# Kernel tuning notes

Hardware: AMD Instinct MI355X
Metric: run time of the kernel (lower is better)

The kernel has to match this reference:

```python
import jax, jax.numpy as jnp
import numpy as np
import math

D_MODEL = 768
N_HEAD = 12
SEQ_LEN = 2048
BATCH = 4


def setup_inputs() -> dict:
    key = jax.random.key(0)
    ks = jax.random.split(key, 5)
    x = jax.random.normal(ks[0], (BATCH, SEQ_LEN, D_MODEL), dtype=jnp.float32)
    s = 1.0 / math.sqrt(D_MODEL)
    W_attn = jax.random.uniform(ks[1], (D_MODEL, 3 * D_MODEL), minval=-s, maxval=s, dtype=jnp.float32)
    b_attn = jax.random.uniform(ks[2], (3 * D_MODEL,), minval=-s, maxval=s, dtype=jnp.float32)
    W_proj = jax.random.uniform(ks[3], (D_MODEL, D_MODEL), minval=-s, maxval=s, dtype=jnp.float32)
    b_proj = jax.random.uniform(ks[4], (D_MODEL,), minval=-s, maxval=s, dtype=jnp.float32)
    return {"x": x, "W_attn": W_attn, "b_attn": b_attn, "W_proj": W_proj, "b_proj": b_proj}


def reference(x, W_attn, b_attn, W_proj, b_proj):
    B, T, C = x.shape
    H = N_HEAD
    hd = C // H
    qkv = x @ W_attn + b_attn  # [B,T,3C]
    q, k, v = jnp.split(qkv, 3, axis=-1)
    # [B,H,T,hd]
    q = q.reshape(B, T, H, hd).transpose(0, 2, 1, 3)
    k = k.reshape(B, T, H, hd).transpose(0, 2, 1, 3)
    v = v.reshape(B, T, H, hd).transpose(0, 2, 1, 3)
    att = jnp.einsum('bhqd,bhkd->bhqk', q, k) * (1.0 / math.sqrt(hd))  # [B,H,T,T]
    causal = jnp.tril(jnp.ones((T, T), dtype=bool))
    att = jnp.where(causal[None, None, :, :], att, -jnp.inf)
    att = jax.nn.softmax(att, axis=-1)
    # attn_pdrop = resid_pdrop = 0.0 -> dropout is identity
    y = jnp.einsum('bhqk,bhkd->bhqd', att, v)  # [B,H,T,hd]
    y = y.transpose(0, 2, 1, 3).reshape(B, T, C)
    return y @ W_proj + b_proj
```

## Files before the change

kernel.cpp:

```cpp
#include <hip/hip_runtime.h>
#include <hip/hip_bf16.h>
#include <math.h>

#define D_MODEL 768
#define N_HEAD  12
#define SEQ     2048
#define BATCH   4
#define HD      64
#define BH      (BATCH*N_HEAD)

typedef __bf16 bf16;
typedef __bf16 bf16x4 __attribute__((ext_vector_type(4)));
typedef __bf16 bf16x8 __attribute__((ext_vector_type(8)));
typedef float  f32x4  __attribute__((ext_vector_type(4)));
typedef float  f32x16 __attribute__((ext_vector_type(16)));
typedef unsigned int u32;

__device__ __forceinline__ f32x4 mfma16(bf16x8 a, bf16x8 b, f32x4 c) {
    return __builtin_amdgcn_mfma_f32_16x16x32_bf16(a, b, c, 0, 0, 0);
}
__device__ __forceinline__ f32x16 mfma32(bf16x8 a, bf16x8 b, f32x16 c) {
    return __builtin_amdgcn_mfma_f32_32x32x16_bf16(a, b, c, 0, 0, 0);
}

__device__ __forceinline__ void gload16(const void* g, void* l) {
    __builtin_amdgcn_global_load_lds((const __attribute__((address_space(1))) u32*)g,
                                     (__attribute__((address_space(3))) u32*)l, 16, 0, 0);
}

__global__ void cvt_bf16(const float* __restrict__ in, bf16* __restrict__ out, int n) {
    int i = (blockIdx.x * blockDim.x + threadIdx.x) * 4;
    if (i < n) {
        float4 v = *(const float4*)(in + i);
        bf16x4 o;
        o[0] = (bf16)v.x; o[1] = (bf16)v.y; o[2] = (bf16)v.z; o[3] = (bf16)v.w;
        *(bf16x4*)(out + i) = o;
    }
}

__global__ __launch_bounds__(256)
void transpose_cvt(const float* __restrict__ in, bf16* __restrict__ out, int R, int C) {
    __shared__ float tile[64][65];
    int tid = threadIdx.x;
    int tr = blockIdx.y * 64, tc = blockIdx.x * 64;
    int r0 = tid >> 4, c0 = (tid & 15) * 4;
    #pragma unroll
    for (int i = 0; i < 4; ++i) {
        float4 v = *(const float4*)&in[(long)(tr + r0 + i * 16) * C + tc + c0];
        tile[r0 + i * 16][c0 + 0] = v.x;
        tile[r0 + i * 16][c0 + 1] = v.y;
        tile[r0 + i * 16][c0 + 2] = v.z;
        tile[r0 + i * 16][c0 + 3] = v.w;
    }
    __syncthreads();
    int orr = (tid & 15) * 4;
    #pragma unroll
    for (int i = 0; i < 4; ++i) {
        int oc = (tid >> 4) + i * 16;
        bf16x4 o;
        #pragma unroll
        for (int j = 0; j < 4; ++j) o[j] = (bf16)tile[orr + j][oc];
        *(bf16x4*)&out[(long)(tc + oc) * R + tr + orr] = o;
    }
}

template<int MODE>
__global__ __launch_bounds__(256)
void gemm_bt(const bf16* __restrict__ A, const bf16* __restrict__ Bt,
             const float* __restrict__ bias,
             bf16* __restrict__ qo, bf16* __restrict__ ko, bf16* __restrict__ vto,
             float* __restrict__ outf,
             int M, int N, int K) {
    __shared__ bf16 As[128 * 32];
    __shared__ bf16 Bs[128 * 32];
    int tid = threadIdx.x;
    int wave = tid >> 6, lane = tid & 63;
    int wr = wave >> 1, wc = wave & 1;
    int lq = lane >> 4, lc = lane & 15;
    int mbase = blockIdx.x * 128, nbase = blockIdx.y * 128;
    int srow = wave * 32 + (lane >> 2), scol = (lane & 3) * 8;
    const bf16* aS = A  + (long)(mbase + srow) * K + scol;
    const bf16* bS = Bt + (long)(nbase + srow) * K + scol;
    char* AsB = (char*)As + wave * 2048;
    char* BsB = (char*)Bs + wave * 2048;
    f32x4 acc[4][4] = {};
    for (int kt = 0; kt < K; kt += 32) {
        gload16(aS + kt,                AsB);
        gload16(aS + 16 * (long)K + kt, AsB + 1024);
        gload16(bS + kt,                BsB);
        gload16(bS + 16 * (long)K + kt, BsB + 1024);
        __syncthreads();
        bf16x8 af[4], bfr[4];
        #pragma unroll
        for (int mf = 0; mf < 4; ++mf)
            af[mf]  = *(const bf16x8*)((char*)As + (wr * 64 + mf * 16 + lc) * 64 + lq * 16);
        #pragma unroll
        for (int nf = 0; nf < 4; ++nf)
            bfr[nf] = *(const bf16x8*)((char*)Bs + (wc * 64 + nf * 16 + lc) * 64 + lq * 16);
        __builtin_amdgcn_s_setprio(1);
        #pragma unroll
        for (int mf = 0; mf < 4; ++mf)
            #pragma unroll
            for (int nf = 0; nf < 4; ++nf)
                acc[mf][nf] = mfma16(af[mf], bfr[nf], acc[mf][nf]);
        __builtin_amdgcn_s_setprio(0);
        __syncthreads();
    }
    #pragma unroll
    for (int mf = 0; mf < 4; ++mf) {
        #pragma unroll
        for (int nf = 0; nf < 4; ++nf) {
            int n = nbase + wc * 64 + nf * 16 + lc;
            float bv = bias[n];
            int m0 = mbase + wr * 64 + mf * 16 + lq * 4;
            if (MODE == 0) {
                int sect = n / 768, cc = n % 768;
                int h = cc >> 6, d = cc & 63;
                int b = m0 >> 11, t0 = m0 & 2047;
                long bh = (long)b * N_HEAD + h;
                if (sect == 0) {
                    #pragma unroll
                    for (int r = 0; r < 4; ++r)
                        qo[(bh * SEQ + t0 + r) * HD + d] = (bf16)((acc[mf][nf][r] + bv) * 0.18033688f);
                } else if (sect == 1) {
                    #pragma unroll
                    for (int r = 0; r < 4; ++r)
                        ko[(bh * SEQ + t0 + r) * HD + d] = (bf16)(acc[mf][nf][r] + bv);
                } else {
                    bf16x4 o;
                    #pragma unroll
                    for (int r = 0; r < 4; ++r) o[r] = (bf16)(acc[mf][nf][r] + bv);
                    *(bf16x4*)&vto[(bh * HD + d) * SEQ + t0] = o;
                }
            } else {
                #pragma unroll
                for (int r = 0; r < 4; ++r)
                    outf[(long)(m0 + r) * N + n] = acc[mf][nf][r] + bv;
            }
        }
    }
}

__global__ __launch_bounds__(256, 4)
void attn_kernel(const bf16* __restrict__ qg, const bf16* __restrict__ kg,
                 const bf16* __restrict__ vtg, bf16* __restrict__ yg) {
    __shared__ __align__(16) bf16 KV[4][64 * 64];
    int tid = threadIdx.x;
    int wave = tid >> 6, lane = tid & 63;
    int q5 = lane & 31, h = lane >> 5;
    int bh = blockIdx.x;
    int tau = gridDim.y - 1 - blockIdx.y;
    int b = bh / N_HEAD, hh = bh % N_HEAD;
    int rh = wave & 1, wp = wave >> 1;
    int nkt  = tau + 1;
    int half = nkt >> 1;
    int base = wp ? half : 0;
    int cnt  = wp ? nkt - half : half;
    int maxc = nkt - half;
    long koff = (long)bh * SEQ * HD;
    long voff = (long)bh * HD * SEQ;
    int qrow = tau * 64 + rh * 32 + q5;

    bf16x8 qf[4];
    #pragma unroll
    for (int s = 0; s < 4; ++s)
        qf[s] = *(const bf16x8*)&qg[koff + (long)qrow * HD + s * 16 + h * 8];

    f32x16 y0 = {}, y1 = {};
    float m2 = -INFINITY, lsum = 0.f;

    int srow0 = rh * 32 + (lane >> 3);
    int scolsw = ((lane & 7) ^ (lane >> 3)) << 3;
    int rsw = lane & 7;
    const char* KsC = (const char*)KV[2 * wp];
    const char* VsC = (const char*)KV[2 * wp + 1];

    for (int i = 0; i < maxc; ++i) {
        int tt = base + i;
        bool active = i < cnt;
        if (active) {
            int k0 = tt * 64;
            char* KsB = (char*)KV[2 * wp]     + rh * 4096;
            char* VsB = (char*)KV[2 * wp + 1] + rh * 4096;
            #pragma unroll
            for (int j = 0; j < 4; ++j) {
                gload16(kg + koff + (long)(k0 + srow0 + j * 8) * HD + scolsw,  KsB + j * 1024);
                gload16(vtg + voff + (long)(srow0 + j * 8) * SEQ + k0 + scolsw, VsB + j * 1024);
            }
        }
        __syncthreads();
        if (active) {
            int k0 = tt * 64;
            f32x16 s0 = {}, s1 = {};
            __builtin_amdgcn_s_setprio(1);
            #pragma unroll
            for (int s = 0; s < 4; ++s) {
                bf16x8 kf0 = *(const bf16x8*)(KsC + q5 * 128        + (((s * 2 + h) ^ rsw) << 4));
                bf16x8 kf1 = *(const bf16x8*)(KsC + (32 + q5) * 128 + (((s * 2 + h) ^ rsw) << 4));
                s0 = mfma32(kf0, qf[s], s0);
                s1 = mfma32(kf1, qf[s], s1);
            }
            __builtin_amdgcn_s_setprio(0);
            if (tt == nkt - 1) {
                #pragma unroll
                for (int r = 0; r < 16; ++r) {
                    int ka = k0 + (r & 3) + 8 * (r >> 2) + 4 * h;
                    if (ka > qrow)      s0[r] = -INFINITY;
                    if (ka + 32 > qrow) s1[r] = -INFINITY;
                }
            }
            float pmax = s0[0];
            #pragma unroll
            for (int r = 1; r < 16; ++r) pmax = fmaxf(pmax, s0[r]);
            #pragma unroll
            for (int r = 0; r < 16; ++r) pmax = fmaxf(pmax, s1[r]);
            pmax = fmaxf(pmax, __shfl_xor(pmax, 32));
            if (!__all(pmax <= m2 + 11.5f)) {
                float mnew = fmaxf(m2, pmax);
                float sc = __builtin_amdgcn_exp2f(m2 - mnew);
                #pragma unroll
                for (int r = 0; r < 16; ++r) { y0[r] *= sc; y1[r] *= sc; }
                lsum *= sc;
                m2 = mnew;
            }
            float psum = 0.f;
            u32 d0a[4], d1a[4], d0b[4], d1b[4];
            #pragma unroll
            for (int m = 0; m < 4; ++m) {
                union { bf16x4 v; u32 w[2]; } pa, pb;
                #pragma unroll
                for (int rr = 0; rr < 4; ++rr) {
                    float p0 = __builtin_amdgcn_exp2f(s0[4 * m + rr] - m2);
                    float p1 = __builtin_amdgcn_exp2f(s1[4 * m + rr] - m2);
                    psum += p0 + p1;
                    pa.v[rr] = (bf16)p0; pb.v[rr] = (bf16)p1;
                }
                d0a[m] = pa.w[0]; d1a[m] = pa.w[1];
                d0b[m] = pb.w[0]; d1b[m] = pb.w[1];
            }
            psum += __shfl_xor(psum, 32);
            lsum += psum;
            u32 e0a[4], e1a[4], e0b[4], e1b[4];
            #pragma unroll
            for (int m = 0; m < 4; ++m) {
                e0a[m] = __shfl_xor(d0a[m], 32); e1a[m] = __shfl_xor(d1a[m], 32);
                e0b[m] = __shfl_xor(d0b[m], 32); e1b[m] = __shfl_xor(d1b[m], 32);
            }
            __builtin_amdgcn_s_setprio(1);
            #pragma unroll
            for (int s = 0; s < 4; ++s) {
                int m0 = 2 * (s & 1), m1 = m0 + 1;
                union { bf16x8 v; u32 w[4]; } fr;
                if (s < 2) {
                    fr.w[0] = h ? e0a[m1] : d0a[m0];
                    fr.w[1] = h ? e1a[m1] : d1a[m0];
                    fr.w[2] = h ? d0a[m1] : e0a[m0];
                    fr.w[3] = h ? d1a[m1] : e1a[m0];
                } else {
                    fr.w[0] = h ? e0b[m1] : d0b[m0];
                    fr.w[1] = h ? e1b[m1] : d1b[m0];
                    fr.w[2] = h ? d0b[m1] : e0b[m0];
                    fr.w[3] = h ? d1b[m1] : e1b[m0];
                }
                bf16x8 v0 = *(const bf16x8*)(VsC + q5 * 128        + (((s * 2 + h) ^ rsw) << 4));
                bf16x8 v1 = *(const bf16x8*)(VsC + (32 + q5) * 128 + (((s * 2 + h) ^ rsw) << 4));
                y0 = mfma32(v0, fr.v, y0);
                y1 = mfma32(v1, fr.v, y1);
            }
            __builtin_amdgcn_s_setprio(0);
        }
        __syncthreads();
    }

    float* ms = (float*)&KV[0][0];
    int slot = (rh * 64 + lane) * 36;
    if (wp) {
        ms[slot] = m2; ms[slot + 1] = lsum;
        #pragma unroll
        for (int r = 0; r < 16; ++r) { ms[slot + 4 + r] = y0[r]; ms[slot + 20 + r] = y1[r]; }
    }
    __syncthreads();
    if (!wp) {
        float mB = ms[slot], lB = ms[slot + 1];
        float mf = fmaxf(m2, mB);
        float a  = __builtin_amdgcn_exp2f(m2 - mf);
        float bb = __builtin_amdgcn_exp2f(mB - mf);
        float inv = 1.f / (lsum * a + lB * bb);
        long rowoff = ((long)b * SEQ + qrow) * D_MODEL + (long)hh * HD;
        #pragma unroll
        for (int m = 0; m < 4; ++m) {
            bf16x4 o0, o1;
            #pragma unroll
            for (int rr = 0; rr < 4; ++rr) {
                o0[rr] = (bf16)((y0[4 * m + rr] * a + ms[slot + 4 + 4 * m + rr] * bb) * inv);
                o1[rr] = (bf16)((y1[4 * m + rr] * a + ms[slot + 20 + 4 * m + rr] * bb) * inv);
            }
            *(bf16x4*)&yg[rowoff + 8 * m + 4 * h]      = o0;
            *(bf16x4*)&yg[rowoff + 32 + 8 * m + 4 * h] = o1;
        }
    }
}

extern "C" void kernel_launch(void* const* d_in, const int* in_sizes, int n_in,
                              void* d_out, int out_size, void* d_ws, size_t ws_size,
                              hipStream_t stream) {
    const float* x      = (const float*)d_in[0];
    const float* W_attn = (const float*)d_in[1];
    const float* b_attn = (const float*)d_in[2];
    const float* W_proj = (const float*)d_in[3];
    const float* b_proj = (const float*)d_in[4];
    float* out = (float*)d_out;

    char* ws = (char*)d_ws;
    size_t off = 0;
    auto alloc = [&](size_t bytes) { void* p = ws + off; off += (bytes + 255) & ~255ULL; return p; };
    bf16* xb  = (bf16*)alloc(8192ULL * 768 * 2);
    bf16* Wab = (bf16*)alloc(2304ULL * 768 * 2);
    bf16* Wpb = (bf16*)alloc(768ULL * 768 * 2);
    bf16* qb_ = (bf16*)alloc((size_t)BH * SEQ * HD * 2);
    bf16* kb_ = (bf16*)alloc((size_t)BH * SEQ * HD * 2);
    bf16* vtb = (bf16*)alloc((size_t)BH * SEQ * HD * 2);
    bf16* yb  = (bf16*)alloc(8192ULL * 768 * 2);

    hipLaunchKernelGGL(cvt_bf16, dim3((8192 * 768 / 4 + 255) / 256), dim3(256), 0, stream,
                       x, xb, 8192 * 768);
    hipLaunchKernelGGL(transpose_cvt, dim3(2304 / 64, 768 / 64), dim3(256), 0, stream,
                       W_attn, Wab, 768, 2304);
    hipLaunchKernelGGL(transpose_cvt, dim3(768 / 64, 768 / 64), dim3(256), 0, stream,
                       W_proj, Wpb, 768, 768);
    hipLaunchKernelGGL((gemm_bt<0>), dim3(64, 18), dim3(256), 0, stream,
                       xb, Wab, b_attn, qb_, kb_, vtb, (float*)nullptr, 8192, 2304, 768);
    hipLaunchKernelGGL(attn_kernel, dim3(48, 32), dim3(256), 0, stream,
                       qb_, kb_, vtb, yb);
    hipLaunchKernelGGL((gemm_bt<1>), dim3(64, 6), dim3(256), 0, stream,
                       yb, Wpb, b_proj, (bf16*)nullptr, (bf16*)nullptr, (bf16*)nullptr, out, 8192, 768, 768);
}
```

Measured before the change: 208.5 us.

## Merge prep kernels and double GEMM K-tile with XOR-swizzled LDS

Three prep launches (the x cast and two weight transpose-casts) are merged into one kernel that picks its role from the block index, saving two launches. The GEMM K-tile grows from 32 to 64, which halves the barrier pairs per K loop. LDS rows are XOR-swizzled on both the global-to-LDS store and the fragment reads to avoid bank conflicts. LDS use doubles to 32KB per block, which may reduce occupancy.

```diff
diff --git a/kernel.cpp b/kernel.cpp
--- a/kernel.cpp
+++ b/kernel.cpp
@@ -28,21 +28,25 @@
                                      (__attribute__((address_space(3))) u32*)l, 16, 0, 0);
 }
 
-__global__ void cvt_bf16(const float* __restrict__ in, bf16* __restrict__ out, int n) {
-    int i = (blockIdx.x * blockDim.x + threadIdx.x) * 4;
-    if (i < n) {
-        float4 v = *(const float4*)(in + i);
+__global__ __launch_bounds__(256)
+void prep(const float* __restrict__ x, const float* __restrict__ Wa, const float* __restrict__ Wp,
+          bf16* __restrict__ xb, bf16* __restrict__ Wab, bf16* __restrict__ Wpb) {
+    __shared__ float tile[64][65];
+    int blk = blockIdx.x, tid = threadIdx.x;
+    if (blk < 6144) {
+        int i = (blk * 256 + tid) * 4;
+        float4 v = *(const float4*)(x + i);
         bf16x4 o;
         o[0] = (bf16)v.x; o[1] = (bf16)v.y; o[2] = (bf16)v.z; o[3] = (bf16)v.w;
-        *(bf16x4*)(out + i) = o;
-    }
-}
-
-__global__ __launch_bounds__(256)
-void transpose_cvt(const float* __restrict__ in, bf16* __restrict__ out, int R, int C) {
-    __shared__ float tile[64][65];
-    int tid = threadIdx.x;
-    int tr = blockIdx.y * 64, tc = blockIdx.x * 64;
+        *(bf16x4*)(xb + i) = o;
+        return;
+    }
+    const float* in; bf16* out; int C; int tile_id;
+    if (blk < 6576) { in = Wa; out = Wab; C = 2304; tile_id = blk - 6144; }
+    else            { in = Wp; out = Wpb; C = 768;  tile_id = blk - 6576; }
+    const int R = 768;
+    int tpr = C / 64;
+    int tr = (tile_id / tpr) * 64, tc = (tile_id % tpr) * 64;
     int r0 = tid >> 4, c0 = (tid & 15) * 4;
     #pragma unroll
     for (int i = 0; i < 4; ++i) {
@@ -71,39 +75,48 @@
              bf16* __restrict__ qo, bf16* __restrict__ ko, bf16* __restrict__ vto,
              float* __restrict__ outf,
              int M, int N, int K) {
-    __shared__ bf16 As[128 * 32];
-    __shared__ bf16 Bs[128 * 32];
+    __shared__ bf16 As[128 * 64];
+    __shared__ bf16 Bs[128 * 64];
     int tid = threadIdx.x;
     int wave = tid >> 6, lane = tid & 63;
     int wr = wave >> 1, wc = wave & 1;
     int lq = lane >> 4, lc = lane & 15;
     int mbase = blockIdx.x * 128, nbase = blockIdx.y * 128;
-    int srow = wave * 32 + (lane >> 2), scol = (lane & 3) * 8;
+    int srow = wave * 32 + (lane >> 3);
+    int scol = ((lane & 7) ^ (lane >> 3)) << 3;
     const bf16* aS = A  + (long)(mbase + srow) * K + scol;
     const bf16* bS = Bt + (long)(nbase + srow) * K + scol;
-    char* AsB = (char*)As + wave * 2048;
-    char* BsB = (char*)Bs + wave * 2048;
+    char* AsB = (char*)As + wave * 4096;
+    char* BsB = (char*)Bs + wave * 4096;
     f32x4 acc[4][4] = {};
-    for (int kt = 0; kt < K; kt += 32) {
-        gload16(aS + kt,                AsB);
-        gload16(aS + 16 * (long)K + kt, AsB + 1024);
-        gload16(bS + kt,                BsB);
-        gload16(bS + 16 * (long)K + kt, BsB + 1024);
+    for (int kt = 0; kt < K; kt += 64) {
+        #pragma unroll
+        for (int j = 0; j < 4; ++j) {
+            gload16(aS + kt + (long)j * 8 * K, AsB + j * 1024);
+            gload16(bS + kt + (long)j * 8 * K, BsB + j * 1024);
+        }
         __syncthreads();
-        bf16x8 af[4], bfr[4];
-        #pragma unroll
-        for (int mf = 0; mf < 4; ++mf)
-            af[mf]  = *(const bf16x8*)((char*)As + (wr * 64 + mf * 16 + lc) * 64 + lq * 16);
-        #pragma unroll
-        for (int nf = 0; nf < 4; ++nf)
-            bfr[nf] = *(const bf16x8*)((char*)Bs + (wc * 64 + nf * 16 + lc) * 64 + lq * 16);
-        __builtin_amdgcn_s_setprio(1);
-        #pragma unroll
-        for (int mf = 0; mf < 4; ++mf)
-            #pragma unroll
-            for (int nf = 0; nf < 4; ++nf)
-                acc[mf][nf] = mfma16(af[mf], bfr[nf], acc[mf][nf]);
-        __builtin_amdgcn_s_setprio(0);
+        #pragma unroll
+        for (int ksub = 0; ksub < 2; ++ksub) {
+            bf16x8 af[4], bfr[4];
+            #pragma unroll
+            for (int mf = 0; mf < 4; ++mf) {
+                int R = wr * 64 + mf * 16 + lc;
+                af[mf]  = *(const bf16x8*)((char*)As + R * 128 + (((ksub * 4 + lq) ^ (lc & 7)) << 4));
+            }
+            #pragma unroll
+            for (int nf = 0; nf < 4; ++nf) {
+                int R = wc * 64 + nf * 16 + lc;
+                bfr[nf] = *(const bf16x8*)((char*)Bs + R * 128 + (((ksub * 4 + lq) ^ (lc & 7)) << 4));
+            }
+            __builtin_amdgcn_s_setprio(1);
+            #pragma unroll
+            for (int mf = 0; mf < 4; ++mf)
+                #pragma unroll
+                for (int nf = 0; nf < 4; ++nf)
+                    acc[mf][nf] = mfma16(af[mf], bfr[nf], acc[mf][nf]);
+            __builtin_amdgcn_s_setprio(0);
+        }
         __syncthreads();
     }
     #pragma unroll
@@ -322,12 +335,8 @@
     bf16* vtb = (bf16*)alloc((size_t)BH * SEQ * HD * 2);
     bf16* yb  = (bf16*)alloc(8192ULL * 768 * 2);
 
-    hipLaunchKernelGGL(cvt_bf16, dim3((8192 * 768 / 4 + 255) / 256), dim3(256), 0, stream,
-                       x, xb, 8192 * 768);
-    hipLaunchKernelGGL(transpose_cvt, dim3(2304 / 64, 768 / 64), dim3(256), 0, stream,
-                       W_attn, Wab, 768, 2304);
-    hipLaunchKernelGGL(transpose_cvt, dim3(768 / 64, 768 / 64), dim3(256), 0, stream,
-                       W_proj, Wpb, 768, 768);
+    hipLaunchKernelGGL(prep, dim3(6720), dim3(256), 0, stream,
+                       x, W_attn, W_proj, xb, Wab, Wpb);
     hipLaunchKernelGGL((gemm_bt<0>), dim3(64, 18), dim3(256), 0, stream,
                        xb, Wab, b_attn, qb_, kb_, vtb, (float*)nullptr, 8192, 2304, 768);
     hipLaunchKernelGGL(attn_kernel, dim3(48, 32), dim3(256), 0, stream,
```

New measurement: 191.7 us (median of 2 runs). 8.0% less time.
